# Optimization experiments

Measured on AMD Instinct MI355X. Metric: run time of the kernel, lower is better.

## Reference

```python
import jax, jax.numpy as jnp
import numpy as np

B, T, D, H = 4, 2048, 1024, 16
HD = D // H  # head_dim = 64
ROPE_BASE = 10000.0


def rotate_half(x):
    # Faithful to source: interleaved rotate. x[..., ::2], x[..., 1::2]
    x1 = x[..., ::2]
    x2 = x[..., 1::2]
    return jnp.stack((-x2, x1), axis=-1).reshape(x.shape)


def rope_tables(seq_len, dim, dtype=jnp.float32):
    inv = 1.0 / (ROPE_BASE ** (jnp.arange(0, dim, 2, dtype=jnp.float32) / dim))
    t = jnp.arange(seq_len, dtype=jnp.float32)
    freqs = jnp.einsum('i,j->ij', t, inv)          # [T, dim/2]
    emb = jnp.concatenate((freqs, freqs), axis=-1)  # [T, dim]
    return jnp.cos(emb).astype(dtype)[None, None], jnp.sin(emb).astype(dtype)[None, None]


def setup_inputs() -> dict:
    key = jax.random.key(0)
    ks = jax.random.split(key, 9)
    s = 0.02
    return {
        'x':  jax.random.normal(ks[0], (B, T, D), jnp.float32),
        'Wq': jax.random.normal(ks[1], (D, D), jnp.float32) * s,
        'bq': jnp.zeros((D,), jnp.float32),
        'Wk': jax.random.normal(ks[2], (D, D), jnp.float32) * s,
        'bk': jnp.zeros((D,), jnp.float32),
        'Wv': jax.random.normal(ks[3], (D, D), jnp.float32) * s,
        'bv': jnp.zeros((D,), jnp.float32),
        'Wo': jax.random.normal(ks[4], (D, D), jnp.float32) * s,
        'bo': jnp.zeros((D,), jnp.float32),
    }


def reference(x, Wq, bq, Wk, bk, Wv, bv, Wo, bo):
    b, t, d = x.shape
    # QKV projections -> [B, H, T, HD]
    def proj(W, bias):
        return (x @ W.T + bias).reshape(b, t, H, HD).transpose(0, 2, 1, 3)
    q, k, v = proj(Wq, bq), proj(Wk, bk), proj(Wv, bv)
    # RoPE (as written in source: non-interleaved cos/sin with interleaved rotate_half)
    cos, sin = rope_tables(t, HD, x.dtype)
    q = q * cos + rotate_half(q) * sin
    k = k * cos + rotate_half(k) * sin
    # Attention
    scale = 1.0 / jnp.sqrt(jnp.asarray(HD, x.dtype))
    attn = jnp.einsum('bhqd,bhkd->bhqk', q, k) * scale
    attn = jax.nn.softmax(attn, axis=-1)
    out = jnp.einsum('bhqk,bhkd->bhqd', attn, v)
    out = out.transpose(0, 2, 1, 3).reshape(b, t, d)
    return out @ Wo.T + bo
```

## Files before the change

kernel.cpp:

```cpp
#include <hip/hip_runtime.h>
#include <hip/hip_bf16.h>

constexpr int Bb = 4, Tt = 2048, Dd = 1024, Hh = 16, HD = 64;
constexpr int Mm = Bb * Tt;

typedef __attribute__((ext_vector_type(8))) short bf16x8;
typedef __attribute__((ext_vector_type(4))) short s16x4;
typedef __attribute__((ext_vector_type(4))) float f32x4;
typedef __attribute__((ext_vector_type(16))) float f32x16;

__device__ __forceinline__ short f2bf(float f) {
  union { float f; unsigned u; } v; v.f = f;
  unsigned r = (v.u + 0x7fffu + ((v.u >> 16) & 1u)) >> 16;
  return (short)r;
}

__device__ __forceinline__ unsigned cvt_pk_bf16(float lo, float hi) {
  unsigned r;
  asm("v_cvt_pk_bf16_f32 %0, %1, %2" : "=v"(r) : "v"(lo), "v"(hi));
  return r;
}

__device__ __forceinline__ void gl_lds16(const short* gsrc, short* ldst) {
  __builtin_amdgcn_global_load_lds(
      (const __attribute__((address_space(1))) void*)gsrc,
      (__attribute__((address_space(3))) void*)ldst, 16, 0, 0);
}

__global__ __launch_bounds__(256) void cvt_k(const float* __restrict__ src,
                                             short* __restrict__ dst, int n4) {
  int i = blockIdx.x * 256 + threadIdx.x;
  if (i >= n4) return;
  float4 v = ((const float4*)src)[i];
  s16x4 p = { f2bf(v.x), f2bf(v.y), f2bf(v.z), f2bf(v.w) };
  ((s16x4*)dst)[i] = p;
}

__global__ __launch_bounds__(256) void cvt3_k(
    const float* __restrict__ s0, const float* __restrict__ s1,
    const float* __restrict__ s2,
    short* __restrict__ d0, short* __restrict__ d1, short* __restrict__ d2) {
  const float* src = blockIdx.y == 0 ? s0 : blockIdx.y == 1 ? s1 : s2;
  short* dst = blockIdx.y == 0 ? d0 : blockIdx.y == 1 ? d1 : d2;
  int i = blockIdx.x * 256 + threadIdx.x;
  float4 v = ((const float4*)src)[i];
  s16x4 p = { f2bf(v.x), f2bf(v.y), f2bf(v.z), f2bf(v.w) };
  ((s16x4*)dst)[i] = p;
}

__global__ void rope_tab(float* __restrict__ cs, float* __restrict__ sn) {
  int idx = blockIdx.x * 256 + threadIdx.x;
  if (idx >= Tt * HD) return;
  int t = idx >> 6, d = idx & (HD - 1);
  float f = powf(10000.0f, -(float)(d & 31) / 32.0f);
  float ang = (float)t * f;
  cs[idx] = cosf(ang);
  sn[idx] = sinf(ang);
}

__global__ __launch_bounds__(256) void gemm_qk(
    const short* __restrict__ Ab,
    const short* __restrict__ Wqb, const short* __restrict__ Wkb,
    const float* __restrict__ bq, const float* __restrict__ bk,
    short* __restrict__ Qo, short* __restrict__ Ko,
    const float* __restrict__ cs, const float* __restrict__ sn)
{
  constexpr int K = 1024;
  __shared__ short Alds[128 * 64];
  __shared__ short Blds[128 * 64];
  const bool isQ = (blockIdx.z == 0);
  const short* Wb = isQ ? Wqb : Wkb;
  const float* bias = isQ ? bq : bk;
  short* outb = isQ ? Qo : Ko;
  const float scale = isQ ? 0.18033688f : 1.0f;

  const int tid = threadIdx.x;
  const int lane = tid & 63, wave = tid >> 6;
  const int g = lane >> 4, li = lane & 15;
  const int m0 = blockIdx.x * 128, n0 = blockIdx.y * 128;
  const int wm = (wave >> 1) * 64, wn = (wave & 1) * 64;
  f32x4 acc[4][4] = {};

  const int lrow = lane >> 3;
  const int soff = lrow * K + (((lane & 7) ^ lrow) * 8);
  const short* Asrc = Ab + (size_t)(m0 + wave * 32) * K + soff;
  const short* Bsrc = Wb + (size_t)(n0 + wave * 32) * K + soff;
  short* Adst = Alds + wave * 32 * 64;
  short* Bdst = Blds + wave * 32 * 64;

  for (int k0 = 0; k0 < K; k0 += 64) {
    #pragma unroll
    for (int i = 0; i < 4; i++) {
      gl_lds16(Asrc + (size_t)i * 8 * K + k0, Adst + i * 8 * 64);
      gl_lds16(Bsrc + (size_t)i * 8 * K + k0, Bdst + i * 8 * 64);
    }
    __syncthreads();

    bf16x8 af[4][2], bfr[4][2];
    #pragma unroll
    for (int i = 0; i < 4; i++) {
      int row = wm + i * 16 + li, sw = li & 7;
      #pragma unroll
      for (int kk = 0; kk < 2; kk++)
        af[i][kk] = *(const bf16x8*)&Alds[row * 64 + (((kk * 4 + g) ^ sw) * 8)];
    }
    #pragma unroll
    for (int j = 0; j < 4; j++) {
      int row = wn + j * 16 + li, sw = li & 7;
      #pragma unroll
      for (int kk = 0; kk < 2; kk++)
        bfr[j][kk] = *(const bf16x8*)&Blds[row * 64 + (((kk * 4 + g) ^ sw) * 8)];
    }
    #pragma unroll
    for (int i = 0; i < 4; i++)
      #pragma unroll
      for (int j = 0; j < 4; j++)
        #pragma unroll
        for (int kk = 0; kk < 2; kk++)
          acc[i][j] = __builtin_amdgcn_mfma_f32_16x16x32_bf16(
              af[i][kk], bfr[j][kk], acc[i][j], 0, 0, 0);
    __syncthreads();
  }

  #pragma unroll
  for (int i = 0; i < 4; i++)
    #pragma unroll
    for (int j = 0; j < 4; j++)
      #pragma unroll
      for (int r = 0; r < 4; r++) {
        int m = m0 + wm + i * 16 + g * 4 + r;
        int n = n0 + wn + j * 16 + li;
        float val = acc[i][j][r] + bias[n];
        float partner = __shfl_xor(val, 1, 64);
        int tt = m & (Tt - 1), hd = n & (HD - 1);
        float c = cs[tt * HD + hd], s = sn[tt * HD + hd];
        float rh = (n & 1) ? partner : -partner;
        val = (val * c + rh * s) * scale;
        int bI = m >> 11, h = n >> 6;
        outb[(((size_t)bI * Hh + h) * Tt + tt) * HD + hd] = f2bf(val);
      }
}

__global__ __launch_bounds__(256) void gemm_v(
    const short* __restrict__ Ab, const short* __restrict__ Wvb,
    const float* __restrict__ bias, short* __restrict__ outb)
{
  constexpr int K = 1024;
  __shared__ short Alds[128 * 64];
  __shared__ short Blds[128 * 64];
  const int tid = threadIdx.x;
  const int lane = tid & 63, wave = tid >> 6;
  const int g = lane >> 4, li = lane & 15;
  const int m0 = blockIdx.x * 128, n0 = blockIdx.y * 128;
  const int wm = (wave >> 1) * 64, wn = (wave & 1) * 64;
  f32x4 acc[4][4] = {};

  const int lrow = lane >> 3;
  const int soff = lrow * K + (((lane & 7) ^ lrow) * 8);
  const short* Asrc = Ab + (size_t)(m0 + wave * 32) * K + soff;
  const short* Bsrc = Wvb + (size_t)(n0 + wave * 32) * K + soff;
  short* Adst = Alds + wave * 32 * 64;
  short* Bdst = Blds + wave * 32 * 64;

  for (int k0 = 0; k0 < K; k0 += 64) {
    #pragma unroll
    for (int i = 0; i < 4; i++) {
      gl_lds16(Asrc + (size_t)i * 8 * K + k0, Adst + i * 8 * 64);
      gl_lds16(Bsrc + (size_t)i * 8 * K + k0, Bdst + i * 8 * 64);
    }
    __syncthreads();

    bf16x8 af[4][2], bfr[4][2];
    #pragma unroll
    for (int i = 0; i < 4; i++) {
      int row = wm + i * 16 + li, sw = li & 7;
      #pragma unroll
      for (int kk = 0; kk < 2; kk++)
        af[i][kk] = *(const bf16x8*)&Alds[row * 64 + (((kk * 4 + g) ^ sw) * 8)];
    }
    #pragma unroll
    for (int j = 0; j < 4; j++) {
      int row = wn + j * 16 + li, sw = li & 7;
      #pragma unroll
      for (int kk = 0; kk < 2; kk++)
        bfr[j][kk] = *(const bf16x8*)&Blds[row * 64 + (((kk * 4 + g) ^ sw) * 8)];
    }
    #pragma unroll
    for (int i = 0; i < 4; i++)
      #pragma unroll
      for (int j = 0; j < 4; j++)
        #pragma unroll
        for (int kk = 0; kk < 2; kk++)
          acc[i][j] = __builtin_amdgcn_mfma_f32_16x16x32_bf16(
              af[i][kk], bfr[j][kk], acc[i][j], 0, 0, 0);
    __syncthreads();
  }

  #pragma unroll
  for (int i = 0; i < 4; i++)
    #pragma unroll
    for (int j = 0; j < 4; j++) {
      int n = n0 + wn + j * 16 + li;
      s16x4 pk;
      #pragma unroll
      for (int r = 0; r < 4; r++) pk[r] = f2bf(acc[i][j][r] + bias[n]);
      int mb = m0 + wm + i * 16 + g * 4;
      int bI = mb >> 11, t0 = mb & (Tt - 1), h = n >> 6, d = n & (HD - 1);
      *(s16x4*)(outb + (((size_t)bI * Hh + h) * HD + d) * Tt + t0) = pk;
    }
}

__global__ __launch_bounds__(256) void gemm_fin(
    const short* __restrict__ Ab, const short* __restrict__ Wb,
    const float* __restrict__ bias, float* __restrict__ outf)
{
  constexpr int K = 1024;
  __shared__ short Alds[128 * 64];
  __shared__ short Blds[128 * 64];
  const int tid = threadIdx.x;
  const int lane = tid & 63, wave = tid >> 6;
  const int g = lane >> 4, li = lane & 15;
  const int m0 = blockIdx.x * 128, n0 = blockIdx.y * 128;
  const int wm = (wave >> 1) * 64, wn = (wave & 1) * 64;
  f32x4 acc[4][4] = {};

  const int lrow = lane >> 3;
  const int soff = lrow * K + (((lane & 7) ^ lrow) * 8);
  const short* Asrc = Ab + (size_t)(m0 + wave * 32) * K + soff;
  const short* Bsrc = Wb + (size_t)(n0 + wave * 32) * K + soff;
  short* Adst = Alds + wave * 32 * 64;
  short* Bdst = Blds + wave * 32 * 64;

  for (int k0 = 0; k0 < K; k0 += 64) {
    #pragma unroll
    for (int i = 0; i < 4; i++) {
      gl_lds16(Asrc + (size_t)i * 8 * K + k0, Adst + i * 8 * 64);
      gl_lds16(Bsrc + (size_t)i * 8 * K + k0, Bdst + i * 8 * 64);
    }
    __syncthreads();

    bf16x8 af[4][2], bfr[4][2];
    #pragma unroll
    for (int i = 0; i < 4; i++) {
      int row = wm + i * 16 + li, sw = li & 7;
      #pragma unroll
      for (int kk = 0; kk < 2; kk++)
        af[i][kk] = *(const bf16x8*)&Alds[row * 64 + (((kk * 4 + g) ^ sw) * 8)];
    }
    #pragma unroll
    for (int j = 0; j < 4; j++) {
      int row = wn + j * 16 + li, sw = li & 7;
      #pragma unroll
      for (int kk = 0; kk < 2; kk++)
        bfr[j][kk] = *(const bf16x8*)&Blds[row * 64 + (((kk * 4 + g) ^ sw) * 8)];
    }
    #pragma unroll
    for (int i = 0; i < 4; i++)
      #pragma unroll
      for (int j = 0; j < 4; j++)
        #pragma unroll
        for (int kk = 0; kk < 2; kk++)
          acc[i][j] = __builtin_amdgcn_mfma_f32_16x16x32_bf16(
              af[i][kk], bfr[j][kk], acc[i][j], 0, 0, 0);
    __syncthreads();
  }

  #pragma unroll
  for (int i = 0; i < 4; i++)
    #pragma unroll
    for (int j = 0; j < 4; j++)
      #pragma unroll
      for (int r = 0; r < 4; r++) {
        int m = m0 + wm + i * 16 + g * 4 + r;
        int n = n0 + wn + j * 16 + li;
        outf[(size_t)m * Dd + n] = acc[i][j][r] + bias[n];
      }
}

__device__ __forceinline__ void store_o(const f32x16& o, float inv,
                                        short* __restrict__ AO, size_t rowbase,
                                        int colbase, int h) {
  #pragma unroll
  for (int R = 0; R < 4; R++) {
    s16x4 pk;
    #pragma unroll
    for (int j = 0; j < 4; j++) pk[j] = f2bf(o[R * 4 + j] * inv);
    *(s16x4*)(AO + rowbase + colbase + 8 * R + 4 * h) = pk;
  }
}

__global__ __launch_bounds__(256, 4) void attn_k(
    const short* __restrict__ Qb, const short* __restrict__ Kb,
    const short* __restrict__ Vt_g, short* __restrict__ AO)
{
  __shared__ short Klds[64][72];
  __shared__ short Vt[64][72];
  const int tid = threadIdx.x, lane = tid & 63, wave = tid >> 6;
  const int h = lane >> 5;
  const int ql = lane & 31;
  const int bh = blockIdx.x;
  const int q0 = blockIdx.y * 128 + wave * 32;
  const size_t base  = (size_t)bh * Tt * HD;
  const size_t basev = (size_t)bh * HD * Tt;

  bf16x8 qf[4];
  #pragma unroll
  for (int ks = 0; ks < 4; ks++)
    qf[ks] = *(const bf16x8*)(Qb + base + (size_t)(q0 + ql) * HD + ks * 16 + h * 8);

  float l_i = 0.f;
  f32x16 o0 = {}, o1 = {};

  for (int kv0 = 0; kv0 < Tt; kv0 += 64) {
    #pragma unroll
    for (int s = 0; s < 2; s++) {
      int f = tid + s * 256; int row = f >> 3, c8 = f & 7;
      *(bf16x8*)&Klds[row][c8 * 8] =
          *(const bf16x8*)(Kb + base + (size_t)(kv0 + row) * HD + c8 * 8);
      *(bf16x8*)&Vt[row][c8 * 8] =
          *(const bf16x8*)(Vt_g + basev + (size_t)row * Tt + kv0 + c8 * 8);
    }
    __syncthreads();

    f32x16 st0 = {}, st1 = {};
    __builtin_amdgcn_s_setprio(1);
    #pragma unroll
    for (int ks = 0; ks < 4; ks++) {
      bf16x8 kf0 = *(const bf16x8*)&Klds[ql][ks * 16 + h * 8];
      bf16x8 kf1 = *(const bf16x8*)&Klds[32 + ql][ks * 16 + h * 8];
      st0 = __builtin_amdgcn_mfma_f32_32x32x16_bf16(kf0, qf[ks], st0, 0, 0, 0);
      st1 = __builtin_amdgcn_mfma_f32_32x32x16_bf16(kf1, qf[ks], st1, 0, 0, 0);
    }
    __builtin_amdgcn_s_setprio(0);

    float rs = 0.f;
    #pragma unroll
    for (int r = 0; r < 16; r++) { st0[r] = __builtin_amdgcn_exp2f(st0[r]); rs += st0[r]; }
    #pragma unroll
    for (int r = 0; r < 16; r++) { st1[r] = __builtin_amdgcn_exp2f(st1[r]); rs += st1[r]; }
    l_i += rs;

    __builtin_amdgcn_s_setprio(1);
    #pragma unroll
    for (int ks = 0; ks < 4; ks++) {
      const int b0 = ((2 * ks) & 3) * 4;
      float A0, A1, A2, A3, B0, B1, B2, B3;
      if (ks < 2) {
        A0 = st0[b0]; A1 = st0[b0 + 1]; A2 = st0[b0 + 2]; A3 = st0[b0 + 3];
        B0 = st0[b0 + 4]; B1 = st0[b0 + 5]; B2 = st0[b0 + 6]; B3 = st0[b0 + 7];
      } else {
        A0 = st1[b0]; A1 = st1[b0 + 1]; A2 = st1[b0 + 2]; A3 = st1[b0 + 3];
        B0 = st1[b0 + 4]; B1 = st1[b0 + 5]; B2 = st1[b0 + 6]; B3 = st1[b0 + 7];
      }
      unsigned wa0 = cvt_pk_bf16(A0, A1), wa1 = cvt_pk_bf16(A2, A3);
      unsigned wb0 = cvt_pk_bf16(B0, B1), wb1 = cvt_pk_bf16(B2, B3);
      unsigned s0 = h ? wa0 : wb0, s1 = h ? wa1 : wb1;
      unsigned r0 = (unsigned)__shfl_xor((int)s0, 32, 64);
      unsigned r1 = (unsigned)__shfl_xor((int)s1, 32, 64);
      unsigned own0 = h ? wb0 : wa0, own1 = h ? wb1 : wa1;
      union { unsigned u[4]; bf16x8 v; } pa;
      pa.u[0] = h ? r0 : own0;  pa.u[1] = h ? r1 : own1;
      pa.u[2] = h ? own0 : r0;  pa.u[3] = h ? own1 : r1;

      bf16x8 vf0 = *(const bf16x8*)&Vt[ql][ks * 16 + h * 8];
      bf16x8 vf1 = *(const bf16x8*)&Vt[32 + ql][ks * 16 + h * 8];
      o0 = __builtin_amdgcn_mfma_f32_32x32x16_bf16(vf0, pa.v, o0, 0, 0, 0);
      o1 = __builtin_amdgcn_mfma_f32_32x32x16_bf16(vf1, pa.v, o1, 0, 0, 0);
    }
    __builtin_amdgcn_s_setprio(0);
    __syncthreads();
  }

  float l_tot = l_i + __shfl_xor(l_i, 32, 64);
  float inv = 1.0f / l_tot;
  const int b = bh >> 4, hh = bh & 15;
  size_t rowbase = ((size_t)b * Tt + q0 + ql) * Dd;
  store_o(o0, inv, AO, rowbase, hh * 64 + 0, h);
  store_o(o1, inv, AO, rowbase, hh * 64 + 32, h);
}

extern "C" void kernel_launch(void* const* d_in, const int* in_sizes, int n_in,
                              void* d_out, int out_size, void* d_ws, size_t ws_size,
                              hipStream_t stream)
{
  const float* x  = (const float*)d_in[0];
  const float* Wq = (const float*)d_in[1];
  const float* bq = (const float*)d_in[2];
  const float* Wk = (const float*)d_in[3];
  const float* bk = (const float*)d_in[4];
  const float* Wv = (const float*)d_in[5];
  const float* bv = (const float*)d_in[6];
  const float* Wo = (const float*)d_in[7];
  const float* bo = (const float*)d_in[8];
  float* out = (float*)d_out;

  char* ws = (char*)d_ws;
  float* cs = (float*)ws;
  float* sn = (float*)(ws + (size_t)(1 << 19));
  char*  p0 = ws + ((size_t)1 << 20);
  short* Qb = (short*)(p0);
  short* Kb = (short*)(p0 + ((size_t)16 << 20));
  short* Vb = (short*)(p0 + ((size_t)32 << 20));
  short* xb = (short*)(p0 + ((size_t)48 << 20));
  short* AO  = xb;
  short* Wqb = Vb;
  short* Wkb = (short*)(p0 + ((size_t)34 << 20));
  short* Wob = Kb;
  short* Wvb = (short*)d_out;

  cvt_k<<<dim3(Mm * Dd / 4 / 256), dim3(256), 0, stream>>>(x, xb, Mm * Dd / 4);
  cvt3_k<<<dim3(Dd * Dd / 4 / 256, 3), dim3(256), 0, stream>>>(
      Wq, Wk, Wv, Wqb, Wkb, Wvb);
  rope_tab<<<dim3(512), dim3(256), 0, stream>>>(cs, sn);

  gemm_qk<<<dim3(Mm / 128, Dd / 128, 2), dim3(256), 0, stream>>>(
      xb, Wqb, Wkb, bq, bk, Qb, Kb, cs, sn);
  gemm_v<<<dim3(Mm / 128, Dd / 128), dim3(256), 0, stream>>>(xb, Wvb, bv, Vb);

  attn_k<<<dim3(Bb * Hh, Tt / 128), dim3(256), 0, stream>>>(Qb, Kb, Vb, AO);

  cvt_k<<<dim3(Dd * Dd / 4 / 256), dim3(256), 0, stream>>>(Wo, Wob, Dd * Dd / 4);
  gemm_fin<<<dim3(Mm / 128, Dd / 128), dim3(256), 0, stream>>>(AO, Wob, bo, out);
}
```

Measured before the change: 196.1 us.

## Double KV tile to 128 and compute softmax row sums via ones-MFMA

Each iteration now stages 128 keys and values in LDS instead of 64, halving the number of barrier pairs and load phases per block. The per-lane scalar row-sum accumulation and final cross-half shuffle are replaced by an extra MFMA against a matrix of ones, so the denominator is produced on the matrix unit. This adds a third MFMA per PV step and uses the bf16-rounded probabilities for the sum, which is consistent with the numerator. LDS use per block roughly doubles, which may limit occupancy at four blocks per CU.

```diff
diff --git a/kernel.cpp b/kernel.cpp
--- a/kernel.cpp
+++ b/kernel.cpp
@@ -293,8 +293,8 @@
     const short* __restrict__ Qb, const short* __restrict__ Kb,
     const short* __restrict__ Vt_g, short* __restrict__ AO)
 {
-  __shared__ short Klds[64][72];
-  __shared__ short Vt[64][72];
+  __shared__ short Klds[128][72];
+  __shared__ short Vt[64][136];
   const int tid = threadIdx.x, lane = tid & 63, wave = tid >> 6;
   const int h = lane >> 5;
   const int ql = lane & 31;
@@ -308,71 +308,77 @@
   for (int ks = 0; ks < 4; ks++)
     qf[ks] = *(const bf16x8*)(Qb + base + (size_t)(q0 + ql) * HD + ks * 16 + h * 8);
 
-  float l_i = 0.f;
-  f32x16 o0 = {}, o1 = {};
-
-  for (int kv0 = 0; kv0 < Tt; kv0 += 64) {
-    #pragma unroll
-    for (int s = 0; s < 2; s++) {
-      int f = tid + s * 256; int row = f >> 3, c8 = f & 7;
-      *(bf16x8*)&Klds[row][c8 * 8] =
-          *(const bf16x8*)(Kb + base + (size_t)(kv0 + row) * HD + c8 * 8);
-      *(bf16x8*)&Vt[row][c8 * 8] =
-          *(const bf16x8*)(Vt_g + basev + (size_t)row * Tt + kv0 + c8 * 8);
-    }
-    __syncthreads();
-
-    f32x16 st0 = {}, st1 = {};
-    __builtin_amdgcn_s_setprio(1);
-    #pragma unroll
-    for (int ks = 0; ks < 4; ks++) {
-      bf16x8 kf0 = *(const bf16x8*)&Klds[ql][ks * 16 + h * 8];
-      bf16x8 kf1 = *(const bf16x8*)&Klds[32 + ql][ks * 16 + h * 8];
-      st0 = __builtin_amdgcn_mfma_f32_32x32x16_bf16(kf0, qf[ks], st0, 0, 0, 0);
-      st1 = __builtin_amdgcn_mfma_f32_32x32x16_bf16(kf1, qf[ks], st1, 0, 0, 0);
-    }
-    __builtin_amdgcn_s_setprio(0);
-
-    float rs = 0.f;
-    #pragma unroll
-    for (int r = 0; r < 16; r++) { st0[r] = __builtin_amdgcn_exp2f(st0[r]); rs += st0[r]; }
-    #pragma unroll
-    for (int r = 0; r < 16; r++) { st1[r] = __builtin_amdgcn_exp2f(st1[r]); rs += st1[r]; }
-    l_i += rs;
-
-    __builtin_amdgcn_s_setprio(1);
-    #pragma unroll
-    for (int ks = 0; ks < 4; ks++) {
-      const int b0 = ((2 * ks) & 3) * 4;
-      float A0, A1, A2, A3, B0, B1, B2, B3;
-      if (ks < 2) {
-        A0 = st0[b0]; A1 = st0[b0 + 1]; A2 = st0[b0 + 2]; A3 = st0[b0 + 3];
-        B0 = st0[b0 + 4]; B1 = st0[b0 + 5]; B2 = st0[b0 + 6]; B3 = st0[b0 + 7];
-      } else {
-        A0 = st1[b0]; A1 = st1[b0 + 1]; A2 = st1[b0 + 2]; A3 = st1[b0 + 3];
-        B0 = st1[b0 + 4]; B1 = st1[b0 + 5]; B2 = st1[b0 + 6]; B3 = st1[b0 + 7];
+  union { unsigned u[4]; bf16x8 v; } ones;
+  #pragma unroll
+  for (int i = 0; i < 4; i++) ones.u[i] = 0x3F803F80u;
+
+  f32x16 o0 = {}, o1 = {}, o2 = {};
+
+  for (int kv0 = 0; kv0 < Tt; kv0 += 128) {
+    #pragma unroll
+    for (int s = 0; s < 4; s++) {
+      int f = tid + s * 256;
+      int krow = f >> 3, kc8 = f & 7;
+      *(bf16x8*)&Klds[krow][kc8 * 8] =
+          *(const bf16x8*)(Kb + base + (size_t)(kv0 + krow) * HD + kc8 * 8);
+      int vrow = f >> 4, vc16 = f & 15;
+      *(bf16x8*)&Vt[vrow][vc16 * 8] =
+          *(const bf16x8*)(Vt_g + basev + (size_t)vrow * Tt + kv0 + vc16 * 8);
+    }
+    __syncthreads();
+
+    #pragma unroll
+    for (int j = 0; j < 2; j++) {
+      f32x16 st0 = {}, st1 = {};
+      __builtin_amdgcn_s_setprio(1);
+      #pragma unroll
+      for (int ks = 0; ks < 4; ks++) {
+        bf16x8 kf0 = *(const bf16x8*)&Klds[j * 64 + ql][ks * 16 + h * 8];
+        bf16x8 kf1 = *(const bf16x8*)&Klds[j * 64 + 32 + ql][ks * 16 + h * 8];
+        st0 = __builtin_amdgcn_mfma_f32_32x32x16_bf16(kf0, qf[ks], st0, 0, 0, 0);
+        st1 = __builtin_amdgcn_mfma_f32_32x32x16_bf16(kf1, qf[ks], st1, 0, 0, 0);
       }
-      unsigned wa0 = cvt_pk_bf16(A0, A1), wa1 = cvt_pk_bf16(A2, A3);
-      unsigned wb0 = cvt_pk_bf16(B0, B1), wb1 = cvt_pk_bf16(B2, B3);
-      unsigned s0 = h ? wa0 : wb0, s1 = h ? wa1 : wb1;
-      unsigned r0 = (unsigned)__shfl_xor((int)s0, 32, 64);
-      unsigned r1 = (unsigned)__shfl_xor((int)s1, 32, 64);
-      unsigned own0 = h ? wb0 : wa0, own1 = h ? wb1 : wa1;
-      union { unsigned u[4]; bf16x8 v; } pa;
-      pa.u[0] = h ? r0 : own0;  pa.u[1] = h ? r1 : own1;
-      pa.u[2] = h ? own0 : r0;  pa.u[3] = h ? own1 : r1;
-
-      bf16x8 vf0 = *(const bf16x8*)&Vt[ql][ks * 16 + h * 8];
-      bf16x8 vf1 = *(const bf16x8*)&Vt[32 + ql][ks * 16 + h * 8];
-      o0 = __builtin_amdgcn_mfma_f32_32x32x16_bf16(vf0, pa.v, o0, 0, 0, 0);
-      o1 = __builtin_amdgcn_mfma_f32_32x32x16_bf16(vf1, pa.v, o1, 0, 0, 0);
-    }
-    __builtin_amdgcn_s_setprio(0);
+      __builtin_amdgcn_s_setprio(0);
+
+      #pragma unroll
+      for (int r = 0; r < 16; r++) st0[r] = __builtin_amdgcn_exp2f(st0[r]);
+      #pragma unroll
+      for (int r = 0; r < 16; r++) st1[r] = __builtin_amdgcn_exp2f(st1[r]);
+
+      __builtin_amdgcn_s_setprio(1);
+      #pragma unroll
+      for (int ks = 0; ks < 4; ks++) {
+        const int b0 = ((2 * ks) & 3) * 4;
+        float A0, A1, A2, A3, B0, B1, B2, B3;
+        if (ks < 2) {
+          A0 = st0[b0]; A1 = st0[b0 + 1]; A2 = st0[b0 + 2]; A3 = st0[b0 + 3];
+          B0 = st0[b0 + 4]; B1 = st0[b0 + 5]; B2 = st0[b0 + 6]; B3 = st0[b0 + 7];
+        } else {
+          A0 = st1[b0]; A1 = st1[b0 + 1]; A2 = st1[b0 + 2]; A3 = st1[b0 + 3];
+          B0 = st1[b0 + 4]; B1 = st1[b0 + 5]; B2 = st1[b0 + 6]; B3 = st1[b0 + 7];
+        }
+        unsigned wa0 = cvt_pk_bf16(A0, A1), wa1 = cvt_pk_bf16(A2, A3);
+        unsigned wb0 = cvt_pk_bf16(B0, B1), wb1 = cvt_pk_bf16(B2, B3);
+        unsigned s0 = h ? wa0 : wb0, s1 = h ? wa1 : wb1;
+        unsigned r0 = (unsigned)__shfl_xor((int)s0, 32, 64);
+        unsigned r1 = (unsigned)__shfl_xor((int)s1, 32, 64);
+        unsigned own0 = h ? wb0 : wa0, own1 = h ? wb1 : wa1;
+        union { unsigned u[4]; bf16x8 v; } pa;
+        pa.u[0] = h ? r0 : own0;  pa.u[1] = h ? r1 : own1;
+        pa.u[2] = h ? own0 : r0;  pa.u[3] = h ? own1 : r1;
+
+        bf16x8 vf0 = *(const bf16x8*)&Vt[ql][j * 64 + ks * 16 + h * 8];
+        bf16x8 vf1 = *(const bf16x8*)&Vt[32 + ql][j * 64 + ks * 16 + h * 8];
+        o0 = __builtin_amdgcn_mfma_f32_32x32x16_bf16(vf0, pa.v, o0, 0, 0, 0);
+        o1 = __builtin_amdgcn_mfma_f32_32x32x16_bf16(vf1, pa.v, o1, 0, 0, 0);
+        o2 = __builtin_amdgcn_mfma_f32_32x32x16_bf16(ones.v, pa.v, o2, 0, 0, 0);
+      }
+      __builtin_amdgcn_s_setprio(0);
+    }
     __syncthreads();
   }
 
-  float l_tot = l_i + __shfl_xor(l_i, 32, 64);
-  float inv = 1.0f / l_tot;
+  float inv = 1.0f / o2[0];
   const int b = bh >> 4, hh = bh & 15;
   size_t rowbase = ((size_t)b * Tt + q0 + ql) * Dd;
   store_o(o0, inv, AO, rowbase, hh * 64 + 0, h);
```

Result: slower. 224.8 us (+14.6%).
